# Performance work log

Hardware: AMD Instinct MI355X
Metric: run time of the kernel (lower is better)

The kernel has to match this reference:

```python
import jax, jax.numpy as jnp
import numpy as np

T = 100000
HDIM = 16
UDIM = 7
HID = 64
DT = 5.0 / 60.0  # 5 minutes in hours


def setup_inputs() -> dict:
    key = jax.random.key(0)
    ks = jax.random.split(key, 12)

    def lin(k, out_d, in_d):
        # torch nn.Linear default init: U(-1/sqrt(in), 1/sqrt(in)); scale-equivalent gaussian is fine for a numeric reference
        bound = 1.0 / np.sqrt(in_d)
        return jax.random.uniform(k, (out_d, in_d), jnp.float32, -bound, bound)

    return {
        "U": jax.random.normal(ks[0], (T, UDIM), jnp.float32),
        "W1": lin(ks[1], HID, HDIM + UDIM),
        "b1": jnp.zeros((HID,), jnp.float32),
        "W2": lin(ks[2], HID, HID),
        "b2": jnp.zeros((HID,), jnp.float32),
        "W3": lin(ks[3], HDIM, HID),
        "b3": jnp.zeros((HDIM,), jnp.float32),
        "wd": lin(ks[4], 1, HDIM).reshape(HDIM),
        "bd": jnp.zeros((), jnp.float32),
        "wt": lin(ks[5], 1, HDIM).reshape(HDIM),
        "bt": jnp.zeros((), jnp.float32),
        "wc": lin(ks[6], 1, HDIM).reshape(HDIM),
        "bc": jnp.zeros((), jnp.float32),
        "h0": jnp.zeros((HDIM,), jnp.float32),
    }


def reference(U, W1, b1, W2, b2, W3, b3, wd, bd, wt, bt, wc, bc, h0):
    dt = jnp.float32(DT)

    def step(h, u):
        # readout at current state (before the Euler step), matching the torch loop order
        d = h @ wd + bd
        tx = h @ wt + bt
        ll = h @ wc + bc
        x = jnp.concatenate([h, u])                    # (HDIM+UDIM,)
        z = jnp.tanh(W1 @ x + b1)                      # (HID,)
        z = jnp.tanh(W2 @ z + b2)                      # (HID,)
        dh = W3 @ z + b3                               # (HDIM,)
        return h + dh * dt, (d, tx, ll)

    hT, (delay, taxi, loglam) = jax.lax.scan(step, h0, U)
    return delay, taxi, loglam, hT.reshape(1, HDIM)
```

## Files before the change

### kernel.cpp

```cpp
#include <hip/hip_runtime.h>

typedef float v2f __attribute__((ext_vector_type(2)));

#define T_STEPS 100000
#define UDIM 7
#define NCHUNK 1562
#define TAIL 32
#define ZSTR 68
#define ZH (64 * ZSTR)
#define UROWS 65
#define UAB (UROWS * 64)

__device__ __forceinline__ float tanh_fast(float x) {
    float e = __expf(2.0f * x);
    return 1.0f - 2.0f * __builtin_amdgcn_rcpf(e + 1.0f);
}

__device__ __forceinline__ float readlane_f(float v, int l) {
    return __int_as_float(__builtin_amdgcn_readlane(__float_as_int(v), l));
}

template <int CTRL>
__device__ __forceinline__ float dpp_f(float v) {
    return __int_as_float(__builtin_amdgcn_update_dpp(
        0, __float_as_int(v), CTRL, 0xF, 0xF, true));
}

__global__ __launch_bounds__(128) __attribute__((amdgpu_waves_per_eu(1, 1)))
void node_scan(const float* __restrict__ U,
               const float* __restrict__ W1, const float* __restrict__ b1,
               const float* __restrict__ W2, const float* __restrict__ b2,
               const float* __restrict__ W3, const float* __restrict__ b3,
               const float* __restrict__ wd, const float* __restrict__ bd,
               const float* __restrict__ wt, const float* __restrict__ bt,
               const float* __restrict__ wc, const float* __restrict__ bc,
               const float* __restrict__ h0,
               float* __restrict__ out)
{
    const int tid  = threadIdx.x;
    const int wv   = tid >> 6;
    const int lane = tid & 63;
    const int g = lane >> 2;
    const int q = lane & 3;
    const float dt = (float)(5.0 / 60.0);

    __shared__ __align__(16) float zbuf[64];
    __shared__ __align__(16) float ubuf[3 * 512];
    __shared__ __align__(16) float zhist[2 * ZH];
    __shared__ __align__(16) float cbuf[3 * 64];
    __shared__ __align__(16) float uab[2 * UAB];
    __shared__ __align__(16) float Msh[64 * 64];
    __shared__ int flg[4];

    if (tid == 0) { flg[0] = 0; flg[1] = 0; flg[2] = 0; }

    float w1h[16]; float b2r = 0.f;
    v2f W2p[4][8];
    v2f W1up[3]; float W1u6 = 0.f, b1l = 0.f;
    float rbD = 0.f, rbT = 0.f, rbC = 0.f, rchD = 0.f, rchT = 0.f, rchC = 0.f;

    if (wv == 0) {
#pragma unroll
        for (int j = 0; j < 16; ++j) w1h[j] = W1[lane * 23 + j];
        b2r = b2[lane];
#pragma unroll
        for (int d = 0; d < 4; ++d) {
            const int orow = (g << 2) | (q ^ d);
            const float* w2r = W2 + orow * 64 + q * 16;
#pragma unroll
            for (int j = 0; j < 8; ++j) W2p[d][j] = (v2f){ w2r[2 * j], w2r[2 * j + 1] };
        }
        for (int c = 0; c < 64; ++c) {
            float acc = 0.f;
#pragma unroll
            for (int k = 0; k < 16; ++k) acc = fmaf(w1h[k], W3[k * 64 + c], acc);
            Msh[lane * 64 + c] = acc;
        }
    } else {
#pragma unroll
        for (int j = 0; j < 3; ++j) {
            W1up[j].x = W1[lane * 23 + 16 + 2 * j];
            W1up[j].y = W1[lane * 23 + 17 + 2 * j];
        }
        W1u6 = W1[lane * 23 + 22];
        b1l = b1[lane];
        float cd = 0.f, ct = 0.f, cc = 0.f;
        for (int k = 0; k < 16; ++k) {
            const float w3v = W3[k * 64 + lane];
            cd = fmaf(wd[k], w3v, cd);
            ct = fmaf(wt[k], w3v, ct);
            cc = fmaf(wc[k], w3v, cc);
        }
        cbuf[lane] = cd; cbuf[64 + lane] = ct; cbuf[128 + lane] = cc;
        rchD = bd[0]; rchT = bt[0]; rchC = bc[0];
        for (int k = 0; k < 16; ++k) {
            rbD = fmaf(wd[k], b3[k], rbD);  rchD = fmaf(wd[k], h0[k], rchD);
            rbT = fmaf(wt[k], b3[k], rbT);  rchT = fmaf(wt[k], h0[k], rchT);
            rbC = fmaf(wc[k], b3[k], rbC);  rchC = fmaf(wc[k], h0[k], rchC);
        }
        rbD *= dt; rbT *= dt; rbC *= dt;
#pragma unroll
        for (int c = 0; c < 3; ++c) {
            const int base = c * 448, dst = c * 512;
#pragma unroll
            for (int r = 0; r < UDIM; ++r) {
                int flat = r * 64 + lane;
                int s = flat / 7, cc2 = flat % 7;
                ubuf[dst + s * 8 + cc2] = U[base + flat];
            }
            ubuf[dst + lane * 8 + 7] = 0.f;
        }
    }
    __syncthreads();

    if (wv == 0) {
        v2f Mp[4][8];
#pragma unroll
        for (int d = 0; d < 4; ++d) {
            const int orow = (g << 2) | (q ^ d);
            const float* mr = Msh + orow * 64 + q * 16;
#pragma unroll
            for (int j = 0; j < 8; ++j) Mp[d][j] = (v2f){ mr[2 * j], mr[2 * j + 1] };
        }
        float m3od = 0.f;
#pragma unroll
        for (int k = 0; k < 16; ++k) m3od = fmaf(w1h[k], b3[k], m3od);
        float A = 0.f;
        for (int k = 0; k < 16; ++k) A = fmaf(w1h[k], h0[k], A);

        while (__hip_atomic_load(&flg[1], __ATOMIC_ACQUIRE,
                                 __HIP_MEMORY_SCOPE_WORKGROUP) < 1)
            __builtin_amdgcn_s_sleep(1);
        float uacc = uab[lane];

        auto step = [&](int li, int ub4, int zb4) {
            const float z1 = tanh_fast(A + uacc);
            zbuf[lane] = z1;
            float4 s0 = *(const float4*)&zbuf[q * 16 + 0];
            float4 s1 = *(const float4*)&zbuf[q * 16 + 4];
            float4 s2 = *(const float4*)&zbuf[q * 16 + 8];
            float4 s3 = *(const float4*)&zbuf[q * 16 + 12];
            const float uacc_next = uab[ub4 + (li + 1) * 64 + lane];

            v2f e0 = {s0.x, s0.y}, e1 = {s0.z, s0.w};
            v2f e2 = {s1.x, s1.y}, e3 = {s1.z, s1.w};
            v2f e4 = {s2.x, s2.y}, e5 = {s2.z, s2.w};
            v2f e6 = {s3.x, s3.y}, e7 = {s3.z, s3.w};
            v2f c0 = {b2r, 0.f}, c1 = {0.f, 0.f}, c2 = {0.f, 0.f}, c3 = {0.f, 0.f};
            c0 = __builtin_elementwise_fma(W2p[0][0], e0, c0);
            c1 = __builtin_elementwise_fma(W2p[1][0], e0, c1);
            c2 = __builtin_elementwise_fma(W2p[2][0], e0, c2);
            c3 = __builtin_elementwise_fma(W2p[3][0], e0, c3);
            c0 = __builtin_elementwise_fma(W2p[0][1], e1, c0);
            c1 = __builtin_elementwise_fma(W2p[1][1], e1, c1);
            c2 = __builtin_elementwise_fma(W2p[2][1], e1, c2);
            c3 = __builtin_elementwise_fma(W2p[3][1], e1, c3);
            c0 = __builtin_elementwise_fma(W2p[0][2], e2, c0);
            c1 = __builtin_elementwise_fma(W2p[1][2], e2, c1);
            c2 = __builtin_elementwise_fma(W2p[2][2], e2, c2);
            c3 = __builtin_elementwise_fma(W2p[3][2], e2, c3);
            c0 = __builtin_elementwise_fma(W2p[0][3], e3, c0);
            c1 = __builtin_elementwise_fma(W2p[1][3], e3, c1);
            c2 = __builtin_elementwise_fma(W2p[2][3], e3, c2);
            c3 = __builtin_elementwise_fma(W2p[3][3], e3, c3);
            c0 = __builtin_elementwise_fma(W2p[0][4], e4, c0);
            c1 = __builtin_elementwise_fma(W2p[1][4], e4, c1);
            c2 = __builtin_elementwise_fma(W2p[2][4], e4, c2);
            c3 = __builtin_elementwise_fma(W2p[3][4], e4, c3);
            c0 = __builtin_elementwise_fma(W2p[0][5], e5, c0);
            c1 = __builtin_elementwise_fma(W2p[1][5], e5, c1);
            c2 = __builtin_elementwise_fma(W2p[2][5], e5, c2);
            c3 = __builtin_elementwise_fma(W2p[3][5], e5, c3);
            c0 = __builtin_elementwise_fma(W2p[0][6], e6, c0);
            c1 = __builtin_elementwise_fma(W2p[1][6], e6, c1);
            c2 = __builtin_elementwise_fma(W2p[2][6], e6, c2);
            c3 = __builtin_elementwise_fma(W2p[3][6], e6, c3);
            c0 = __builtin_elementwise_fma(W2p[0][7], e7, c0);
            c1 = __builtin_elementwise_fma(W2p[1][7], e7, c1);
            c2 = __builtin_elementwise_fma(W2p[2][7], e7, c2);
            c3 = __builtin_elementwise_fma(W2p[3][7], e7, c3);
            const float P0 = c0.x + c0.y;
            const float P1 = c1.x + c1.y;
            const float P2 = c2.x + c2.y;
            const float P3 = c3.x + c3.y;
            const float Q = P0 + dpp_f<0xB1>(P1) + dpp_f<0x4E>(P2) + dpp_f<0x1B>(P3);
            const float z2 = tanh_fast(Q);
            zhist[zb4 + li * ZSTR + lane] = z2;
            const float* zrow = &zhist[zb4 + li * ZSTR + q * 16];
            float4 t0 = *(const float4*)&zrow[0];
            float4 t1 = *(const float4*)&zrow[4];
            float4 t2 = *(const float4*)&zrow[8];
            float4 t3 = *(const float4*)&zrow[12];

            v2f f0 = {t0.x, t0.y}, f1 = {t0.z, t0.w};
            v2f f2 = {t1.x, t1.y}, f3 = {t1.z, t1.w};
            v2f f4 = {t2.x, t2.y}, f5 = {t2.z, t2.w};
            v2f f6 = {t3.x, t3.y}, f7 = {t3.z, t3.w};
            v2f m0 = {m3od, 0.f}, m1 = {0.f, 0.f}, m2 = {0.f, 0.f}, m3 = {0.f, 0.f};
            m0 = __builtin_elementwise_fma(Mp[0][0], f0, m0);
            m1 = __builtin_elementwise_fma(Mp[1][0], f0, m1);
            m2 = __builtin_elementwise_fma(Mp[2][0], f0, m2);
            m3 = __builtin_elementwise_fma(Mp[3][0], f0, m3);
            m0 = __builtin_elementwise_fma(Mp[0][1], f1, m0);
            m1 = __builtin_elementwise_fma(Mp[1][1], f1, m1);
            m2 = __builtin_elementwise_fma(Mp[2][1], f1, m2);
            m3 = __builtin_elementwise_fma(Mp[3][1], f1, m3);
            m0 = __builtin_elementwise_fma(Mp[0][2], f2, m0);
            m1 = __builtin_elementwise_fma(Mp[1][2], f2, m1);
            m2 = __builtin_elementwise_fma(Mp[2][2], f2, m2);
            m3 = __builtin_elementwise_fma(Mp[3][2], f2, m3);
            m0 = __builtin_elementwise_fma(Mp[0][3], f3, m0);
            m1 = __builtin_elementwise_fma(Mp[1][3], f3, m1);
            m2 = __builtin_elementwise_fma(Mp[2][3], f3, m2);
            m3 = __builtin_elementwise_fma(Mp[3][3], f3, m3);
            m0 = __builtin_elementwise_fma(Mp[0][4], f4, m0);
            m1 = __builtin_elementwise_fma(Mp[1][4], f4, m1);
            m2 = __builtin_elementwise_fma(Mp[2][4], f4, m2);
            m3 = __builtin_elementwise_fma(Mp[3][4], f4, m3);
            m0 = __builtin_elementwise_fma(Mp[0][5], f5, m0);
            m1 = __builtin_elementwise_fma(Mp[1][5], f5, m1);
            m2 = __builtin_elementwise_fma(Mp[2][5], f5, m2);
            m3 = __builtin_elementwise_fma(Mp[3][5], f5, m3);
            m0 = __builtin_elementwise_fma(Mp[0][6], f6, m0);
            m1 = __builtin_elementwise_fma(Mp[1][6], f6, m1);
            m2 = __builtin_elementwise_fma(Mp[2][6], f6, m2);
            m3 = __builtin_elementwise_fma(Mp[3][6], f6, m3);
            m0 = __builtin_elementwise_fma(Mp[0][7], f7, m0);
            m1 = __builtin_elementwise_fma(Mp[1][7], f7, m1);
            m2 = __builtin_elementwise_fma(Mp[2][7], f7, m2);
            m3 = __builtin_elementwise_fma(Mp[3][7], f7, m3);
            const float R0 = m0.x + m0.y;
            const float R1 = m1.x + m1.y;
            const float R2 = m2.x + m2.y;
            const float R3 = m3.x + m3.y;
            const float R = R0 + dpp_f<0xB1>(R1) + dpp_f<0x4E>(R2) + dpp_f<0x1B>(R3);
            A = fmaf(dt, R, A);
            uacc = uacc_next;
        };

        for (int cb = 0; cb <= NCHUNK; ++cb) {
            while (__hip_atomic_load(&flg[1], __ATOMIC_ACQUIRE,
                                     __HIP_MEMORY_SCOPE_WORKGROUP) < cb + 1)
                __builtin_amdgcn_s_sleep(1);
            while (__hip_atomic_load(&flg[2], __ATOMIC_ACQUIRE,
                                     __HIP_MEMORY_SCOPE_WORKGROUP) < cb - 1)
                __builtin_amdgcn_s_sleep(1);
            const int zb4 = (cb & 1) * ZH;
            const int ub4 = (cb & 1) * UAB;
            if (cb < NCHUNK) {
#pragma unroll 8
                for (int li = 0; li < 64; ++li) step(li, ub4, zb4);
            } else {
                for (int li = 0; li < TAIL; ++li) step(li, ub4, zb4);
            }
            __hip_atomic_store(&flg[0], cb + 1, __ATOMIC_RELEASE,
                               __HIP_MEMORY_SCOPE_WORKGROUP);
        }
    } else {
        float vacc = 0.f;

        auto uacc_chunk = [&](int c) {
            const int par = (c & 1) * UAB;
            const int src = (c % 3) * 512;
            const int nxt = ((c + 1) % 3) * 512;
            for (int li = 0; li < UROWS; ++li) {
                const int uo = (li < 64) ? src + li * 8 : nxt;
                float4 ua = *(const float4*)&ubuf[uo];
                float4 ub = *(const float4*)&ubuf[uo + 4];
                v2f uv = __builtin_elementwise_fma(W1up[0], (v2f){ua.x, ua.y}, (v2f){0.f, 0.f});
                uv = __builtin_elementwise_fma(W1up[1], (v2f){ua.z, ua.w}, uv);
                uv = __builtin_elementwise_fma(W1up[2], (v2f){ub.x, ub.y}, uv);
                uab[par + li * 64 + lane] = uv.x + uv.y + fmaf(W1u6, ub.z, b1l);
            }
        };
        uacc_chunk(0);
        uacc_chunk(1);
        __hip_atomic_store(&flg[1], 2, __ATOMIC_RELEASE,
                           __HIP_MEMORY_SCOPE_WORKGROUP);

        for (int cb = 0; cb <= NCHUNK; ++cb) {
            while (__hip_atomic_load(&flg[0], __ATOMIC_ACQUIRE,
                                     __HIP_MEMORY_SCOPE_WORKGROUP) < cb + 1)
                __builtin_amdgcn_s_sleep(8);
            if (cb + 3 <= NCHUNK) {
                const int dst = ((cb + 3) % 3) * 512;
                const int base = (cb + 3) * 448;
#pragma unroll
                for (int r = 0; r < UDIM; ++r) {
                    int idx = base + r * 64 + lane;
                    if (idx > T_STEPS * UDIM - 1) idx = T_STEPS * UDIM - 1;
                    const float val = U[idx];
                    int flat = r * 64 + lane;
                    int s = flat / 7, c = flat % 7;
                    ubuf[dst + s * 8 + c] = val;
                }
            }
            if (cb + 2 <= NCHUNK) {
                uacc_chunk(cb + 2);
                __hip_atomic_store(&flg[1], cb + 3, __ATOMIC_RELEASE,
                                   __HIP_MEMORY_SCOPE_WORKGROUP);
            }
            const int zb4 = (cb & 1) * ZH;
            const int ns = (cb == NCHUNK) ? TAIL : 64;
            float colsum = 0.f;
            for (int li = 0; li < ns; ++li) colsum += zhist[zb4 + li * ZSTR + lane];
            vacc += colsum;

            const float* zr = &zhist[zb4 + lane * ZSTR];
            v2f sd = {0.f, 0.f}, st = {0.f, 0.f}, sc = {0.f, 0.f};
#pragma unroll
            for (int qq = 0; qq < 32; ++qq) {
                v2f zv = *(const v2f*)&zr[2 * qq];
                sd = __builtin_elementwise_fma(*(const v2f*)&cbuf[2 * qq],       zv, sd);
                st = __builtin_elementwise_fma(*(const v2f*)&cbuf[64 + 2 * qq],  zv, st);
                sc = __builtin_elementwise_fma(*(const v2f*)&cbuf[128 + 2 * qq], zv, sc);
            }
            float Sd = sd.x + sd.y, St = st.x + st.y, Sc = sc.x + sc.y;
            const float oD = Sd, oT = St, oC = Sc;
#pragma unroll
            for (int dl = 1; dl < 64; dl <<= 1) {
                float ud = __shfl_up(Sd, dl, 64);
                float ut = __shfl_up(St, dl, 64);
                float uc = __shfl_up(Sc, dl, 64);
                if (lane >= dl) { Sd += ud; St += ut; Sc += uc; }
            }
            const int t = cb * 64 + lane;
            if (t < T_STEPS) {
                const float fl = (float)lane;
                out[t]               = fmaf(dt, Sd - oD, rchD) + fl * rbD;
                out[T_STEPS + t]     = fmaf(dt, St - oT, rchT) + fl * rbT;
                out[2 * T_STEPS + t] = fmaf(dt, Sc - oC, rchC) + fl * rbC;
            }
            rchD = fmaf(dt, readlane_f(Sd, 63), rchD) + 64.f * rbD;
            rchT = fmaf(dt, readlane_f(St, 63), rchT) + 64.f * rbT;
            rchC = fmaf(dt, readlane_f(Sc, 63), rchC) + 64.f * rbC;
            __hip_atomic_store(&flg[2], cb + 1, __ATOMIC_RELEASE,
                               __HIP_MEMORY_SCOPE_WORKGROUP);
        }

        zbuf[lane] = vacc;
        if (lane < 16) {
            const float* w3r = W3 + lane * 64;
            float h0a = 0.f, h1a = 0.f;
#pragma unroll
            for (int qq = 0; qq < 16; ++qq) {
                float4 za = *(const float4*)&zbuf[qq * 4];
                h0a = fmaf(w3r[4 * qq + 0], za.x, h0a);
                h1a = fmaf(w3r[4 * qq + 1], za.y, h1a);
                h0a = fmaf(w3r[4 * qq + 2], za.z, h0a);
                h1a = fmaf(w3r[4 * qq + 3], za.w, h1a);
            }
            out[3 * T_STEPS + lane] =
                h0[lane] + dt * (h0a + h1a) + (float)T_STEPS * dt * b3[lane];
        }
    }
}

extern "C" void kernel_launch(void* const* d_in, const int* in_sizes, int n_in,
                              void* d_out, int out_size, void* d_ws, size_t ws_size,
                              hipStream_t stream) {
    const float* U  = (const float*)d_in[0];
    const float* W1 = (const float*)d_in[1];
    const float* b1 = (const float*)d_in[2];
    const float* W2 = (const float*)d_in[3];
    const float* b2 = (const float*)d_in[4];
    const float* W3 = (const float*)d_in[5];
    const float* b3 = (const float*)d_in[6];
    const float* wd = (const float*)d_in[7];
    const float* bd = (const float*)d_in[8];
    const float* wt = (const float*)d_in[9];
    const float* bt = (const float*)d_in[10];
    const float* wc = (const float*)d_in[11];
    const float* bc = (const float*)d_in[12];
    const float* h0 = (const float*)d_in[13];
    (void)in_sizes; (void)n_in; (void)out_size; (void)d_ws; (void)ws_size;

    node_scan<<<dim3(1), dim3(128), 0, stream>>>(U, W1, b1, W2, b2, W3, b3,
                                                 wd, bd, wt, bt, wc, bc, h0,
                                                 (float*)d_out);
}
```

Measured before the change: 26.39 ms.

## Replace LDS broadcast of hidden state with DPP row rotations and permlane-swap reductions

Restructures the serial per-step matvecs so each lane keeps a 16-wide row slice and rotates activations within 16-lane rows via DPP instead of writing z1 to LDS and reading it back. Cross-row partial sums are combined with permlane32/16 swaps when available (probed at runtime), with a bpermute/swizzle fallback. The factor of two in tanh's argument is folded into the weights. This aims to shorten the latency-bound per-step critical path by removing LDS round trips, at the cost of extra DPP instructions and a runtime mode check.

```diff
diff --git a/kernel.cpp b/kernel.cpp
--- a/kernel.cpp
+++ b/kernel.cpp
@@ -11,8 +11,14 @@
 #define UROWS 65
 #define UAB (UROWS * 64)
 
-__device__ __forceinline__ float tanh_fast(float x) {
-    float e = __expf(2.0f * x);
+#if __has_builtin(__builtin_amdgcn_permlane32_swap) && __has_builtin(__builtin_amdgcn_permlane16_swap)
+#define HAS_PLSWAP 1
+#else
+#define HAS_PLSWAP 0
+#endif
+
+__device__ __forceinline__ float tanh_pre(float xs) {
+    float e = __expf(xs);
     return 1.0f - 2.0f * __builtin_amdgcn_rcpf(e + 1.0f);
 }
 
@@ -25,6 +31,8 @@
     return __int_as_float(__builtin_amdgcn_update_dpp(
         0, __float_as_int(v), CTRL, 0xF, 0xF, true));
 }
+
+template <int M> struct IC { static constexpr int v = M; };
 
 __global__ __launch_bounds__(128) __attribute__((amdgpu_waves_per_eu(1, 1)))
 void node_scan(const float* __restrict__ U,
@@ -40,8 +48,6 @@
     const int tid  = threadIdx.x;
     const int wv   = tid >> 6;
     const int lane = tid & 63;
-    const int g = lane >> 2;
-    const int q = lane & 3;
     const float dt = (float)(5.0 / 60.0);
 
     __shared__ __align__(16) float zbuf[64];
@@ -54,44 +60,60 @@
 
     if (tid == 0) { flg[0] = 0; flg[1] = 0; flg[2] = 0; }
 
-    float w1h[16]; float b2r = 0.f;
-    v2f W2p[4][8];
+    int dlt = 1, mode = 1;
+    float A = 0.f, m3od = 0.f;
     v2f W1up[3]; float W1u6 = 0.f, b1l = 0.f;
     float rbD = 0.f, rbT = 0.f, rbC = 0.f, rchD = 0.f, rchT = 0.f, rchC = 0.f;
 
     if (wv == 0) {
-#pragma unroll
-        for (int j = 0; j < 16; ++j) w1h[j] = W1[lane * 23 + j];
-        b2r = b2[lane];
-#pragma unroll
-        for (int d = 0; d < 4; ++d) {
-            const int orow = (g << 2) | (q ^ d);
-            const float* w2r = W2 + orow * 64 + q * 16;
-#pragma unroll
-            for (int j = 0; j < 8; ++j) W2p[d][j] = (v2f){ w2r[2 * j], w2r[2 * j + 1] };
-        }
-        for (int c = 0; c < 64; ++c) {
+        const int cl = lane & 15;
+        {
+            float pd = dpp_f<0x121>((float)cl);
+            dlt = ((int)pd - cl) & 15;
+        }
+#if HAS_PLSWAP
+        {
+            auto rp = __builtin_amdgcn_permlane32_swap(lane, 1000 + lane, false, false);
+            auto rq = __builtin_amdgcn_permlane16_swap(lane, 1000 + lane, false, false);
+            bool ok =
+                (int)rp[0] == ((lane & 32) ? 1000 + lane - 32 : lane) &&
+                (int)rp[1] == ((lane & 32) ? 1000 + lane : lane + 32) &&
+                (int)rq[0] == ((lane & 16) ? 1000 + lane - 16 : lane) &&
+                (int)rq[1] == ((lane & 16) ? 1000 + lane : lane + 16);
+            if (__ballot(ok) == ~0ull) mode = 0;
+        }
+#endif
+        float w1h[16];
+#pragma unroll
+        for (int j = 0; j < 16; ++j) w1h[j] = 2.0f * W1[lane * 23 + j];
+        for (int cc = 0; cc < 64; ++cc) {
             float acc = 0.f;
 #pragma unroll
-            for (int k = 0; k < 16; ++k) acc = fmaf(w1h[k], W3[k * 64 + c], acc);
-            Msh[lane * 64 + c] = acc;
-        }
+            for (int k = 0; k < 16; ++k) acc = fmaf(w1h[k], W3[k * 64 + cc], acc);
+            Msh[lane * 64 + cc] = acc;
+        }
+#pragma unroll
+        for (int k = 0; k < 16; ++k) {
+            m3od = fmaf(w1h[k], b3[k], m3od);
+            A    = fmaf(w1h[k], h0[k], A);
+        }
+        zbuf[lane] = m3od;
     } else {
 #pragma unroll
         for (int j = 0; j < 3; ++j) {
-            W1up[j].x = W1[lane * 23 + 16 + 2 * j];
-            W1up[j].y = W1[lane * 23 + 17 + 2 * j];
-        }
-        W1u6 = W1[lane * 23 + 22];
-        b1l = b1[lane];
-        float cd = 0.f, ct = 0.f, cc = 0.f;
+            W1up[j].x = 2.0f * W1[lane * 23 + 16 + 2 * j];
+            W1up[j].y = 2.0f * W1[lane * 23 + 17 + 2 * j];
+        }
+        W1u6 = 2.0f * W1[lane * 23 + 22];
+        b1l = 2.0f * b1[lane];
+        float cd = 0.f, ct = 0.f, ccv = 0.f;
         for (int k = 0; k < 16; ++k) {
             const float w3v = W3[k * 64 + lane];
             cd = fmaf(wd[k], w3v, cd);
             ct = fmaf(wt[k], w3v, ct);
-            cc = fmaf(wc[k], w3v, cc);
-        }
-        cbuf[lane] = cd; cbuf[64 + lane] = ct; cbuf[128 + lane] = cc;
+            ccv = fmaf(wc[k], w3v, ccv);
+        }
+        cbuf[lane] = cd; cbuf[64 + lane] = ct; cbuf[128 + lane] = ccv;
         rchD = bd[0]; rchT = bt[0]; rchC = bc[0];
         for (int k = 0; k < 16; ++k) {
             rbD = fmaf(wd[k], b3[k], rbD);  rchD = fmaf(wd[k], h0[k], rchD);
@@ -103,8 +125,8 @@
         for (int c = 0; c < 3; ++c) {
             const int base = c * 448, dst = c * 512;
 #pragma unroll
-            for (int r = 0; r < UDIM; ++r) {
-                int flat = r * 64 + lane;
+            for (int rr = 0; rr < UDIM; ++rr) {
+                int flat = rr * 64 + lane;
                 int s = flat / 7, cc2 = flat % 7;
                 ubuf[dst + s * 8 + cc2] = U[base + flat];
             }
@@ -114,148 +136,120 @@
     __syncthreads();
 
     if (wv == 0) {
-        v2f Mp[4][8];
-#pragma unroll
-        for (int d = 0; d < 4; ++d) {
-            const int orow = (g << 2) | (q ^ d);
-            const float* mr = Msh + orow * 64 + q * 16;
-#pragma unroll
-            for (int j = 0; j < 8; ++j) Mp[d][j] = (v2f){ mr[2 * j], mr[2 * j + 1] };
-        }
-        float m3od = 0.f;
-#pragma unroll
-        for (int k = 0; k < 16; ++k) m3od = fmaf(w1h[k], b3[k], m3od);
-        float A = 0.f;
-        for (int k = 0; k < 16; ++k) A = fmaf(w1h[k], h0[k], A);
-
-        while (__hip_atomic_load(&flg[1], __ATOMIC_ACQUIRE,
-                                 __HIP_MEMORY_SCOPE_WORKGROUP) < 1)
-            __builtin_amdgcn_s_sleep(1);
-        float uacc = uab[lane];
-
-        auto step = [&](int li, int ub4, int zb4) {
-            const float z1 = tanh_fast(A + uacc);
-            zbuf[lane] = z1;
-            float4 s0 = *(const float4*)&zbuf[q * 16 + 0];
-            float4 s1 = *(const float4*)&zbuf[q * 16 + 4];
-            float4 s2 = *(const float4*)&zbuf[q * 16 + 8];
-            float4 s3 = *(const float4*)&zbuf[q * 16 + 12];
-            const float uacc_next = uab[ub4 + (li + 1) * 64 + lane];
-
-            v2f e0 = {s0.x, s0.y}, e1 = {s0.z, s0.w};
-            v2f e2 = {s1.x, s1.y}, e3 = {s1.z, s1.w};
-            v2f e4 = {s2.x, s2.y}, e5 = {s2.z, s2.w};
-            v2f e6 = {s3.x, s3.y}, e7 = {s3.z, s3.w};
-            v2f c0 = {b2r, 0.f}, c1 = {0.f, 0.f}, c2 = {0.f, 0.f}, c3 = {0.f, 0.f};
-            c0 = __builtin_elementwise_fma(W2p[0][0], e0, c0);
-            c1 = __builtin_elementwise_fma(W2p[1][0], e0, c1);
-            c2 = __builtin_elementwise_fma(W2p[2][0], e0, c2);
-            c3 = __builtin_elementwise_fma(W2p[3][0], e0, c3);
-            c0 = __builtin_elementwise_fma(W2p[0][1], e1, c0);
-            c1 = __builtin_elementwise_fma(W2p[1][1], e1, c1);
-            c2 = __builtin_elementwise_fma(W2p[2][1], e1, c2);
-            c3 = __builtin_elementwise_fma(W2p[3][1], e1, c3);
-            c0 = __builtin_elementwise_fma(W2p[0][2], e2, c0);
-            c1 = __builtin_elementwise_fma(W2p[1][2], e2, c1);
-            c2 = __builtin_elementwise_fma(W2p[2][2], e2, c2);
-            c3 = __builtin_elementwise_fma(W2p[3][2], e2, c3);
-            c0 = __builtin_elementwise_fma(W2p[0][3], e3, c0);
-            c1 = __builtin_elementwise_fma(W2p[1][3], e3, c1);
-            c2 = __builtin_elementwise_fma(W2p[2][3], e3, c2);
-            c3 = __builtin_elementwise_fma(W2p[3][3], e3, c3);
-            c0 = __builtin_elementwise_fma(W2p[0][4], e4, c0);
-            c1 = __builtin_elementwise_fma(W2p[1][4], e4, c1);
-            c2 = __builtin_elementwise_fma(W2p[2][4], e4, c2);
-            c3 = __builtin_elementwise_fma(W2p[3][4], e4, c3);
-            c0 = __builtin_elementwise_fma(W2p[0][5], e5, c0);
-            c1 = __builtin_elementwise_fma(W2p[1][5], e5, c1);
-            c2 = __builtin_elementwise_fma(W2p[2][5], e5, c2);
-            c3 = __builtin_elementwise_fma(W2p[3][5], e5, c3);
-            c0 = __builtin_elementwise_fma(W2p[0][6], e6, c0);
-            c1 = __builtin_elementwise_fma(W2p[1][6], e6, c1);
-            c2 = __builtin_elementwise_fma(W2p[2][6], e6, c2);
-            c3 = __builtin_elementwise_fma(W2p[3][6], e6, c3);
-            c0 = __builtin_elementwise_fma(W2p[0][7], e7, c0);
-            c1 = __builtin_elementwise_fma(W2p[1][7], e7, c1);
-            c2 = __builtin_elementwise_fma(W2p[2][7], e7, c2);
-            c3 = __builtin_elementwise_fma(W2p[3][7], e7, c3);
-            const float P0 = c0.x + c0.y;
-            const float P1 = c1.x + c1.y;
-            const float P2 = c2.x + c2.y;
-            const float P3 = c3.x + c3.y;
-            const float Q = P0 + dpp_f<0xB1>(P1) + dpp_f<0x4E>(P2) + dpp_f<0x1B>(P3);
-            const float z2 = tanh_fast(Q);
-            zhist[zb4 + li * ZSTR + lane] = z2;
-            const float* zrow = &zhist[zb4 + li * ZSTR + q * 16];
-            float4 t0 = *(const float4*)&zrow[0];
-            float4 t1 = *(const float4*)&zrow[4];
-            float4 t2 = *(const float4*)&zrow[8];
-            float4 t3 = *(const float4*)&zrow[12];
-
-            v2f f0 = {t0.x, t0.y}, f1 = {t0.z, t0.w};
-            v2f f2 = {t1.x, t1.y}, f3 = {t1.z, t1.w};
-            v2f f4 = {t2.x, t2.y}, f5 = {t2.z, t2.w};
-            v2f f6 = {t3.x, t3.y}, f7 = {t3.z, t3.w};
-            v2f m0 = {m3od, 0.f}, m1 = {0.f, 0.f}, m2 = {0.f, 0.f}, m3 = {0.f, 0.f};
-            m0 = __builtin_elementwise_fma(Mp[0][0], f0, m0);
-            m1 = __builtin_elementwise_fma(Mp[1][0], f0, m1);
-            m2 = __builtin_elementwise_fma(Mp[2][0], f0, m2);
-            m3 = __builtin_elementwise_fma(Mp[3][0], f0, m3);
-            m0 = __builtin_elementwise_fma(Mp[0][1], f1, m0);
-            m1 = __builtin_elementwise_fma(Mp[1][1], f1, m1);
-            m2 = __builtin_elementwise_fma(Mp[2][1], f1, m2);
-            m3 = __builtin_elementwise_fma(Mp[3][1], f1, m3);
-            m0 = __builtin_elementwise_fma(Mp[0][2], f2, m0);
-            m1 = __builtin_elementwise_fma(Mp[1][2], f2, m1);
-            m2 = __builtin_elementwise_fma(Mp[2][2], f2, m2);
-            m3 = __builtin_elementwise_fma(Mp[3][2], f2, m3);
-            m0 = __builtin_elementwise_fma(Mp[0][3], f3, m0);
-            m1 = __builtin_elementwise_fma(Mp[1][3], f3, m1);
-            m2 = __builtin_elementwise_fma(Mp[2][3], f3, m2);
-            m3 = __builtin_elementwise_fma(Mp[3][3], f3, m3);
-            m0 = __builtin_elementwise_fma(Mp[0][4], f4, m0);
-            m1 = __builtin_elementwise_fma(Mp[1][4], f4, m1);
-            m2 = __builtin_elementwise_fma(Mp[2][4], f4, m2);
-            m3 = __builtin_elementwise_fma(Mp[3][4], f4, m3);
-            m0 = __builtin_elementwise_fma(Mp[0][5], f5, m0);
-            m1 = __builtin_elementwise_fma(Mp[1][5], f5, m1);
-            m2 = __builtin_elementwise_fma(Mp[2][5], f5, m2);
-            m3 = __builtin_elementwise_fma(Mp[3][5], f5, m3);
-            m0 = __builtin_elementwise_fma(Mp[0][6], f6, m0);
-            m1 = __builtin_elementwise_fma(Mp[1][6], f6, m1);
-            m2 = __builtin_elementwise_fma(Mp[2][6], f6, m2);
-            m3 = __builtin_elementwise_fma(Mp[3][6], f6, m3);
-            m0 = __builtin_elementwise_fma(Mp[0][7], f7, m0);
-            m1 = __builtin_elementwise_fma(Mp[1][7], f7, m1);
-            m2 = __builtin_elementwise_fma(Mp[2][7], f7, m2);
-            m3 = __builtin_elementwise_fma(Mp[3][7], f7, m3);
-            const float R0 = m0.x + m0.y;
-            const float R1 = m1.x + m1.y;
-            const float R2 = m2.x + m2.y;
-            const float R3 = m3.x + m3.y;
-            const float R = R0 + dpp_f<0xB1>(R1) + dpp_f<0x4E>(R2) + dpp_f<0x1B>(R3);
-            A = fmaf(dt, R, A);
-            uacc = uacc_next;
+        const int r  = lane >> 4;
+        const int cl = lane & 15;
+
+        auto runw0 = [&](auto MC) {
+            constexpr int MODE = decltype(MC)::v;
+            v2f W2f[4][8], Mf[4][8];
+            float b2v[4], m3v[4];
+            {
+                int offA = 0, offB = (15 * dlt) & 15;
+#pragma unroll
+                for (int s = 0; s < 8; ++s) {
+                    const int kA = (r << 4) | ((cl + offA) & 15);
+                    const int kB = (r << 4) | ((cl + offB) & 15);
+#pragma unroll
+                    for (int d = 0; d < 4; ++d) {
+                        const int o = ((MODE ? (r ^ d) : d) << 4) | cl;
+                        W2f[d][s] = (v2f){2.0f * W2[o * 64 + kA], 2.0f * W2[o * 64 + kB]};
+                        Mf[d][s]  = (v2f){Msh[o * 64 + kA], Msh[o * 64 + kB]};
+                    }
+                    offA = (offA + 2 * dlt) & 15;
+                    offB = (offB + 2 * dlt) & 15;
+                }
+#pragma unroll
+                for (int d = 0; d < 4; ++d) {
+                    if (MODE == 0) {
+                        b2v[d] = (r == 0) ? 2.0f * b2[(d << 4) | cl] : 0.f;
+                        m3v[d] = (r == 0) ? zbuf[(d << 4) | cl] : 0.f;
+                    } else {
+                        b2v[d] = (d == 0) ? 2.0f * b2[lane] : 0.f;
+                        m3v[d] = (d == 0) ? m3od : 0.f;
+                    }
+                }
+            }
+
+            auto combine = [&](v2f a0, v2f a1, v2f a2, v2f a3) -> float {
+                float P0 = a0.x + a0.y, P1 = a1.x + a1.y;
+                float P2 = a2.x + a2.y, P3 = a3.x + a3.y;
+#if HAS_PLSWAP
+                if constexpr (MODE == 0) {
+                    auto rA = __builtin_amdgcn_permlane32_swap(__float_as_int(P0), __float_as_int(P2), false, false);
+                    auto rB = __builtin_amdgcn_permlane32_swap(__float_as_int(P1), __float_as_int(P3), false, false);
+                    float U02 = __int_as_float((int)rA[0]) + __int_as_float((int)rA[1]);
+                    float U13 = __int_as_float((int)rB[0]) + __int_as_float((int)rB[1]);
+                    auto sA = __builtin_amdgcn_permlane16_swap(__float_as_int(U02), __float_as_int(U02), false, false);
+                    auto sB = __builtin_amdgcn_permlane16_swap(__float_as_int(U13), __float_as_int(U13), false, false);
+                    float V02 = __int_as_float((int)sA[0]) + __int_as_float((int)sA[1]);
+                    float V13 = __int_as_float((int)sB[0]) + __int_as_float((int)sB[1]);
+                    return (lane & 16) ? V13 : V02;
+                }
+#endif
+                {
+                    float q0 = P0 + __int_as_float(__builtin_amdgcn_ds_bpermute((lane ^ 32) << 2, __float_as_int(P2)));
+                    float q1 = P1 + __int_as_float(__builtin_amdgcn_ds_bpermute((lane ^ 32) << 2, __float_as_int(P3)));
+                    return q0 + __int_as_float(__builtin_amdgcn_ds_swizzle(__float_as_int(q1), 0x401F));
+                }
+            };
+
+            while (__hip_atomic_load(&flg[1], __ATOMIC_ACQUIRE,
+                                     __HIP_MEMORY_SCOPE_WORKGROUP) < 1)
+                __builtin_amdgcn_s_sleep(1);
+            float uacc = uab[lane];
+
+            auto step = [&](int li, int ub4, int zb4) {
+                const float z1 = tanh_pre(A + uacc);
+                const float uacc_next = uab[ub4 + (li + 1) * 64 + lane];
+                v2f zp; zp.x = z1; zp.y = dpp_f<0x12F>(z1);
+                v2f a0 = {b2v[0], 0.f}, a1 = {b2v[1], 0.f};
+                v2f a2 = {b2v[2], 0.f}, a3 = {b2v[3], 0.f};
+#pragma unroll
+                for (int s = 0; s < 8; ++s) {
+                    a0 = __builtin_elementwise_fma(W2f[0][s], zp, a0);
+                    a1 = __builtin_elementwise_fma(W2f[1][s], zp, a1);
+                    a2 = __builtin_elementwise_fma(W2f[2][s], zp, a2);
+                    a3 = __builtin_elementwise_fma(W2f[3][s], zp, a3);
+                    if (s < 7) { zp.x = dpp_f<0x122>(zp.x); zp.y = dpp_f<0x122>(zp.y); }
+                }
+                const float z2 = tanh_pre(combine(a0, a1, a2, a3));
+                zhist[zb4 + li * ZSTR + lane] = z2;
+                v2f wp; wp.x = z2; wp.y = dpp_f<0x12F>(z2);
+                v2f m0 = {m3v[0], 0.f}, m1 = {m3v[1], 0.f};
+                v2f m2 = {m3v[2], 0.f}, m3r = {m3v[3], 0.f};
+#pragma unroll
+                for (int s = 0; s < 8; ++s) {
+                    m0  = __builtin_elementwise_fma(Mf[0][s], wp, m0);
+                    m1  = __builtin_elementwise_fma(Mf[1][s], wp, m1);
+                    m2  = __builtin_elementwise_fma(Mf[2][s], wp, m2);
+                    m3r = __builtin_elementwise_fma(Mf[3][s], wp, m3r);
+                    if (s < 7) { wp.x = dpp_f<0x122>(wp.x); wp.y = dpp_f<0x122>(wp.y); }
+                }
+                A = fmaf(dt, combine(m0, m1, m2, m3r), A);
+                uacc = uacc_next;
+            };
+
+            for (int cb = 0; cb <= NCHUNK; ++cb) {
+                while (__hip_atomic_load(&flg[1], __ATOMIC_ACQUIRE,
+                                         __HIP_MEMORY_SCOPE_WORKGROUP) < cb + 1)
+                    __builtin_amdgcn_s_sleep(1);
+                while (__hip_atomic_load(&flg[2], __ATOMIC_ACQUIRE,
+                                         __HIP_MEMORY_SCOPE_WORKGROUP) < cb - 1)
+                    __builtin_amdgcn_s_sleep(1);
+                const int zb4 = (cb & 1) * ZH;
+                const int ub4 = (cb & 1) * UAB;
+                if (cb < NCHUNK) {
+#pragma unroll 4
+                    for (int li = 0; li < 64; ++li) step(li, ub4, zb4);
+                } else {
+#pragma unroll 4
+                    for (int li = 0; li < TAIL; ++li) step(li, ub4, zb4);
+                }
+                __hip_atomic_store(&flg[0], cb + 1, __ATOMIC_RELEASE,
+                                   __HIP_MEMORY_SCOPE_WORKGROUP);
+            }
         };
-
-        for (int cb = 0; cb <= NCHUNK; ++cb) {
-            while (__hip_atomic_load(&flg[1], __ATOMIC_ACQUIRE,
-                                     __HIP_MEMORY_SCOPE_WORKGROUP) < cb + 1)
-                __builtin_amdgcn_s_sleep(1);
-            while (__hip_atomic_load(&flg[2], __ATOMIC_ACQUIRE,
-                                     __HIP_MEMORY_SCOPE_WORKGROUP) < cb - 1)
-                __builtin_amdgcn_s_sleep(1);
-            const int zb4 = (cb & 1) * ZH;
-            const int ub4 = (cb & 1) * UAB;
-            if (cb < NCHUNK) {
-#pragma unroll 8
-                for (int li = 0; li < 64; ++li) step(li, ub4, zb4);
-            } else {
-                for (int li = 0; li < TAIL; ++li) step(li, ub4, zb4);
-            }
-            __hip_atomic_store(&flg[0], cb + 1, __ATOMIC_RELEASE,
-                               __HIP_MEMORY_SCOPE_WORKGROUP);
-        }
+        if (mode == 0) runw0(IC<0>{}); else runw0(IC<1>{});
     } else {
         float vacc = 0.f;
 
@@ -286,11 +280,11 @@
                 const int dst = ((cb + 3) % 3) * 512;
                 const int base = (cb + 3) * 448;
 #pragma unroll
-                for (int r = 0; r < UDIM; ++r) {
-                    int idx = base + r * 64 + lane;
+                for (int rr = 0; rr < UDIM; ++rr) {
+                    int idx = base + rr * 64 + lane;
                     if (idx > T_STEPS * UDIM - 1) idx = T_STEPS * UDIM - 1;
                     const float val = U[idx];
-                    int flat = r * 64 + lane;
+                    int flat = rr * 64 + lane;
                     int s = flat / 7, c = flat % 7;
                     ubuf[dst + s * 8 + c] = val;
                 }
```

New measurement: 28.41 ms. +7.6%, slower.

## Fold tanh doubling and dt into weights, rebalance reductions, raise wave priority

Applied to the files above, without the earlier changes.

Pre-scales W1, b1, W2 and b2 by 2 so each tanh skips a multiply, and folds dt into the precomputed M matrix and bias so the state update becomes a plain add. Precomputes A+u ahead of the next step. Reassociates the DPP reduction sums into a tree to shorten the dependency chain on the serial critical path. Raises the compute wave's scheduling priority and widens the readout loop to float4 LDS loads. This slightly changes floating-point rounding.

```diff
diff --git a/kernel.cpp b/kernel.cpp
--- a/kernel.cpp
+++ b/kernel.cpp
@@ -11,8 +11,8 @@
 #define UROWS 65
 #define UAB (UROWS * 64)
 
-__device__ __forceinline__ float tanh_fast(float x) {
-    float e = __expf(2.0f * x);
+__device__ __forceinline__ float tanh_pre(float xs) {
+    float e = __expf(xs);
     return 1.0f - 2.0f * __builtin_amdgcn_rcpf(e + 1.0f);
 }
 
@@ -61,14 +61,15 @@
 
     if (wv == 0) {
 #pragma unroll
-        for (int j = 0; j < 16; ++j) w1h[j] = W1[lane * 23 + j];
-        b2r = b2[lane];
+        for (int j = 0; j < 16; ++j) w1h[j] = 2.0f * W1[lane * 23 + j];
+        b2r = 2.0f * b2[lane];
 #pragma unroll
         for (int d = 0; d < 4; ++d) {
             const int orow = (g << 2) | (q ^ d);
             const float* w2r = W2 + orow * 64 + q * 16;
 #pragma unroll
-            for (int j = 0; j < 8; ++j) W2p[d][j] = (v2f){ w2r[2 * j], w2r[2 * j + 1] };
+            for (int j = 0; j < 8; ++j)
+                W2p[d][j] = (v2f){ 2.0f * w2r[2 * j], 2.0f * w2r[2 * j + 1] };
         }
         for (int c = 0; c < 64; ++c) {
             float acc = 0.f;
@@ -79,11 +80,11 @@
     } else {
 #pragma unroll
         for (int j = 0; j < 3; ++j) {
-            W1up[j].x = W1[lane * 23 + 16 + 2 * j];
-            W1up[j].y = W1[lane * 23 + 17 + 2 * j];
-        }
-        W1u6 = W1[lane * 23 + 22];
-        b1l = b1[lane];
+            W1up[j].x = 2.0f * W1[lane * 23 + 16 + 2 * j];
+            W1up[j].y = 2.0f * W1[lane * 23 + 17 + 2 * j];
+        }
+        W1u6 = 2.0f * W1[lane * 23 + 22];
+        b1l = 2.0f * b1[lane];
         float cd = 0.f, ct = 0.f, cc = 0.f;
         for (int k = 0; k < 16; ++k) {
             const float w3v = W3[k * 64 + lane];
@@ -114,27 +115,30 @@
     __syncthreads();
 
     if (wv == 0) {
+        __builtin_amdgcn_s_setprio(3);
         v2f Mp[4][8];
 #pragma unroll
         for (int d = 0; d < 4; ++d) {
             const int orow = (g << 2) | (q ^ d);
             const float* mr = Msh + orow * 64 + q * 16;
 #pragma unroll
-            for (int j = 0; j < 8; ++j) Mp[d][j] = (v2f){ mr[2 * j], mr[2 * j + 1] };
+            for (int j = 0; j < 8; ++j)
+                Mp[d][j] = (v2f){ dt * mr[2 * j], dt * mr[2 * j + 1] };
         }
         float m3od = 0.f;
 #pragma unroll
         for (int k = 0; k < 16; ++k) m3od = fmaf(w1h[k], b3[k], m3od);
+        m3od *= dt;
         float A = 0.f;
         for (int k = 0; k < 16; ++k) A = fmaf(w1h[k], h0[k], A);
 
         while (__hip_atomic_load(&flg[1], __ATOMIC_ACQUIRE,
                                  __HIP_MEMORY_SCOPE_WORKGROUP) < 1)
             __builtin_amdgcn_s_sleep(1);
-        float uacc = uab[lane];
+        float Az = A + uab[lane];
 
         auto step = [&](int li, int ub4, int zb4) {
-            const float z1 = tanh_fast(A + uacc);
+            const float z1 = tanh_pre(Az);
             zbuf[lane] = z1;
             float4 s0 = *(const float4*)&zbuf[q * 16 + 0];
             float4 s1 = *(const float4*)&zbuf[q * 16 + 4];
@@ -183,8 +187,8 @@
             const float P1 = c1.x + c1.y;
             const float P2 = c2.x + c2.y;
             const float P3 = c3.x + c3.y;
-            const float Q = P0 + dpp_f<0xB1>(P1) + dpp_f<0x4E>(P2) + dpp_f<0x1B>(P3);
-            const float z2 = tanh_fast(Q);
+            const float Q = (P0 + dpp_f<0xB1>(P1)) + (dpp_f<0x4E>(P2) + dpp_f<0x1B>(P3));
+            const float z2 = tanh_pre(Q);
             zhist[zb4 + li * ZSTR + lane] = z2;
             const float* zrow = &zhist[zb4 + li * ZSTR + q * 16];
             float4 t0 = *(const float4*)&zrow[0];
@@ -233,9 +237,9 @@
             const float R1 = m1.x + m1.y;
             const float R2 = m2.x + m2.y;
             const float R3 = m3.x + m3.y;
-            const float R = R0 + dpp_f<0xB1>(R1) + dpp_f<0x4E>(R2) + dpp_f<0x1B>(R3);
-            A = fmaf(dt, R, A);
-            uacc = uacc_next;
+            const float R = (R0 + dpp_f<0xB1>(R1)) + (dpp_f<0x4E>(R2) + dpp_f<0x1B>(R3));
+            A = A + R;
+            Az = A + uacc_next;
         };
 
         for (int cb = 0; cb <= NCHUNK; ++cb) {
@@ -309,11 +313,18 @@
             const float* zr = &zhist[zb4 + lane * ZSTR];
             v2f sd = {0.f, 0.f}, st = {0.f, 0.f}, sc = {0.f, 0.f};
 #pragma unroll
-            for (int qq = 0; qq < 32; ++qq) {
-                v2f zv = *(const v2f*)&zr[2 * qq];
-                sd = __builtin_elementwise_fma(*(const v2f*)&cbuf[2 * qq],       zv, sd);
-                st = __builtin_elementwise_fma(*(const v2f*)&cbuf[64 + 2 * qq],  zv, st);
-                sc = __builtin_elementwise_fma(*(const v2f*)&cbuf[128 + 2 * qq], zv, sc);
+            for (int qq = 0; qq < 16; ++qq) {
+                float4 zv4 = *(const float4*)&zr[4 * qq];
+                float4 cd4 = *(const float4*)&cbuf[4 * qq];
+                float4 ct4 = *(const float4*)&cbuf[64 + 4 * qq];
+                float4 cc4 = *(const float4*)&cbuf[128 + 4 * qq];
+                v2f zlo = {zv4.x, zv4.y}, zhi = {zv4.z, zv4.w};
+                sd = __builtin_elementwise_fma((v2f){cd4.x, cd4.y}, zlo, sd);
+                sd = __builtin_elementwise_fma((v2f){cd4.z, cd4.w}, zhi, sd);
+                st = __builtin_elementwise_fma((v2f){ct4.x, ct4.y}, zlo, st);
+                st = __builtin_elementwise_fma((v2f){ct4.z, ct4.w}, zhi, st);
+                sc = __builtin_elementwise_fma((v2f){cc4.x, cc4.y}, zlo, sc);
+                sc = __builtin_elementwise_fma((v2f){cc4.z, cc4.w}, zhi, sc);
             }
             float Sd = sd.x + sd.y, St = st.x + st.y, Sc = sc.x + sc.y;
             const float oD = Sd, oT = St, oC = Sc;
```

New measurement: 26.66 ms. Within noise of the previous version (+1.0%).

## Replace LDS broadcast of hidden activations with permlane/DPP butterfly exchange

Applied to the files above, without the earlier changes.

On the serial recurrence wave, each step used to broadcast z1 and z2 through LDS (a store followed by float4 reloads). Where the permlane32/16 swap builtins exist, it now gathers 16 values per lane with cross-lane permutes and DPP row rotates. The W2 and M weight registers are permuted to match, and a runtime check confirms the gathered indices cover the quad, falling back to the LDS path otherwise. The aim is to cut LDS round-trip latency from the critical dependency chain, at the cost of more permute instructions and code duplication.

```diff
diff --git a/kernel.cpp b/kernel.cpp
--- a/kernel.cpp
+++ b/kernel.cpp
@@ -11,6 +11,12 @@
 #define UROWS 65
 #define UAB (UROWS * 64)
 
+#if __has_builtin(__builtin_amdgcn_permlane32_swap) && __has_builtin(__builtin_amdgcn_permlane16_swap)
+#define HAS_PLSWAP 1
+#else
+#define HAS_PLSWAP 0
+#endif
+
 __device__ __forceinline__ float tanh_fast(float x) {
     float e = __expf(2.0f * x);
     return 1.0f - 2.0f * __builtin_amdgcn_rcpf(e + 1.0f);
@@ -25,6 +31,28 @@
     return __int_as_float(__builtin_amdgcn_update_dpp(
         0, __float_as_int(v), CTRL, 0xF, 0xF, true));
 }
+
+template <int CTRL>
+__device__ __forceinline__ int dpp_i(int v) {
+    return __builtin_amdgcn_update_dpp(0, v, CTRL, 0xF, 0xF, true);
+}
+
+#if HAS_PLSWAP
+__device__ __forceinline__ void bfly16(int v, int c[16]) {
+    auto p  = __builtin_amdgcn_permlane32_swap(v, v, false, false);
+    auto qa = __builtin_amdgcn_permlane16_swap(p[0], p[0], false, false);
+    auto qb = __builtin_amdgcn_permlane16_swap(p[1], p[1], false, false);
+    int a0 = qa[0], a1 = qa[1], a2 = qb[0], a3 = qb[1];
+    int b0 = dpp_i<0x128>(a0), b1 = dpp_i<0x128>(a1);
+    int b2 = dpp_i<0x128>(a2), b3 = dpp_i<0x128>(a3);
+    c[0] = a0;  c[1] = a1;  c[2] = a2;  c[3] = a3;
+    c[4] = b0;  c[5] = b1;  c[6] = b2;  c[7] = b3;
+    c[8]  = dpp_i<0x124>(a0);  c[9]  = dpp_i<0x124>(a1);
+    c[10] = dpp_i<0x124>(a2);  c[11] = dpp_i<0x124>(a3);
+    c[12] = dpp_i<0x124>(b0);  c[13] = dpp_i<0x124>(b1);
+    c[14] = dpp_i<0x124>(b2);  c[15] = dpp_i<0x124>(b3);
+}
+#endif
 
 __global__ __launch_bounds__(128) __attribute__((amdgpu_waves_per_eu(1, 1)))
 void node_scan(const float* __restrict__ U,
@@ -56,19 +84,48 @@
 
     float w1h[16]; float b2r = 0.f;
     v2f W2p[4][8];
+    int idx[16]; bool fastok = false;
     v2f W1up[3]; float W1u6 = 0.f, b1l = 0.f;
     float rbD = 0.f, rbT = 0.f, rbC = 0.f, rchD = 0.f, rchT = 0.f, rchC = 0.f;
 
     if (wv == 0) {
+#if HAS_PLSWAP
+        {
+            int c[16];
+            bfly16(lane, c);
+            unsigned mlo = 0, mhi = 0;
+#pragma unroll
+            for (int r = 0; r < 16; ++r) {
+                idx[r] = c[r] & 63;
+                if (idx[r] < 32) mlo |= (1u << idx[r]);
+                else             mhi |= (1u << (idx[r] - 32));
+            }
+            unsigned ulo = mlo, uhi = mhi;
+            ulo |= (unsigned)dpp_i<0xB1>((int)mlo);
+            ulo |= (unsigned)dpp_i<0x4E>((int)mlo);
+            ulo |= (unsigned)dpp_i<0x1B>((int)mlo);
+            uhi |= (unsigned)dpp_i<0xB1>((int)mhi);
+            uhi |= (unsigned)dpp_i<0x4E>((int)mhi);
+            uhi |= (unsigned)dpp_i<0x1B>((int)mhi);
+            bool ok = (ulo == 0xFFFFFFFFu) && (uhi == 0xFFFFFFFFu);
+            fastok = (__ballot(ok) == ~0ull);
+        }
+#endif
+        if (!fastok) {
+#pragma unroll
+            for (int r = 0; r < 16; ++r) idx[r] = (q << 4) | r;
+        }
+
 #pragma unroll
         for (int j = 0; j < 16; ++j) w1h[j] = W1[lane * 23 + j];
         b2r = b2[lane];
 #pragma unroll
         for (int d = 0; d < 4; ++d) {
             const int orow = (g << 2) | (q ^ d);
-            const float* w2r = W2 + orow * 64 + q * 16;
-#pragma unroll
-            for (int j = 0; j < 8; ++j) W2p[d][j] = (v2f){ w2r[2 * j], w2r[2 * j + 1] };
+            const float* w2r = W2 + orow * 64;
+#pragma unroll
+            for (int j = 0; j < 8; ++j)
+                W2p[d][j] = (v2f){ w2r[idx[2 * j]], w2r[idx[2 * j + 1]] };
         }
         for (int c = 0; c < 64; ++c) {
             float acc = 0.f;
@@ -118,9 +175,10 @@
 #pragma unroll
         for (int d = 0; d < 4; ++d) {
             const int orow = (g << 2) | (q ^ d);
-            const float* mr = Msh + orow * 64 + q * 16;
-#pragma unroll
-            for (int j = 0; j < 8; ++j) Mp[d][j] = (v2f){ mr[2 * j], mr[2 * j + 1] };
+            const float* mr = Msh + orow * 64;
+#pragma unroll
+            for (int j = 0; j < 8; ++j)
+                Mp[d][j] = (v2f){ mr[idx[2 * j]], mr[idx[2 * j + 1]] };
         }
         float m3od = 0.f;
 #pragma unroll
@@ -133,19 +191,8 @@
             __builtin_amdgcn_s_sleep(1);
         float uacc = uab[lane];
 
-        auto step = [&](int li, int ub4, int zb4) {
-            const float z1 = tanh_fast(A + uacc);
-            zbuf[lane] = z1;
-            float4 s0 = *(const float4*)&zbuf[q * 16 + 0];
-            float4 s1 = *(const float4*)&zbuf[q * 16 + 4];
-            float4 s2 = *(const float4*)&zbuf[q * 16 + 8];
-            float4 s3 = *(const float4*)&zbuf[q * 16 + 12];
-            const float uacc_next = uab[ub4 + (li + 1) * 64 + lane];
-
-            v2f e0 = {s0.x, s0.y}, e1 = {s0.z, s0.w};
-            v2f e2 = {s1.x, s1.y}, e3 = {s1.z, s1.w};
-            v2f e4 = {s2.x, s2.y}, e5 = {s2.z, s2.w};
-            v2f e6 = {s3.x, s3.y}, e7 = {s3.z, s3.w};
+        auto mat2 = [&](v2f e0, v2f e1, v2f e2, v2f e3,
+                        v2f e4, v2f e5, v2f e6, v2f e7) -> float {
             v2f c0 = {b2r, 0.f}, c1 = {0.f, 0.f}, c2 = {0.f, 0.f}, c3 = {0.f, 0.f};
             c0 = __builtin_elementwise_fma(W2p[0][0], e0, c0);
             c1 = __builtin_elementwise_fma(W2p[1][0], e0, c1);
@@ -183,19 +230,10 @@
             const float P1 = c1.x + c1.y;
             const float P2 = c2.x + c2.y;
             const float P3 = c3.x + c3.y;
-            const float Q = P0 + dpp_f<0xB1>(P1) + dpp_f<0x4E>(P2) + dpp_f<0x1B>(P3);
-            const float z2 = tanh_fast(Q);
-            zhist[zb4 + li * ZSTR + lane] = z2;
-            const float* zrow = &zhist[zb4 + li * ZSTR + q * 16];
-            float4 t0 = *(const float4*)&zrow[0];
-            float4 t1 = *(const float4*)&zrow[4];
-            float4 t2 = *(const float4*)&zrow[8];
-            float4 t3 = *(const float4*)&zrow[12];
-
-            v2f f0 = {t0.x, t0.y}, f1 = {t0.z, t0.w};
-            v2f f2 = {t1.x, t1.y}, f3 = {t1.z, t1.w};
-            v2f f4 = {t2.x, t2.y}, f5 = {t2.z, t2.w};
-            v2f f6 = {t3.x, t3.y}, f7 = {t3.z, t3.w};
+            return P0 + dpp_f<0xB1>(P1) + dpp_f<0x4E>(P2) + dpp_f<0x1B>(P3);
+        };
+        auto mat3 = [&](v2f f0, v2f f1, v2f f2, v2f f3,
+                        v2f f4, v2f f5, v2f f6, v2f f7) -> float {
             v2f m0 = {m3od, 0.f}, m1 = {0.f, 0.f}, m2 = {0.f, 0.f}, m3 = {0.f, 0.f};
             m0 = __builtin_elementwise_fma(Mp[0][0], f0, m0);
             m1 = __builtin_elementwise_fma(Mp[1][0], f0, m1);
@@ -233,28 +271,109 @@
             const float R1 = m1.x + m1.y;
             const float R2 = m2.x + m2.y;
             const float R3 = m3.x + m3.y;
-            const float R = R0 + dpp_f<0xB1>(R1) + dpp_f<0x4E>(R2) + dpp_f<0x1B>(R3);
+            return R0 + dpp_f<0xB1>(R1) + dpp_f<0x4E>(R2) + dpp_f<0x1B>(R3);
+        };
+
+#if HAS_PLSWAP
+        auto stepF = [&](int li, int ub4, int zb4) {
+            const float z1 = tanh_fast(A + uacc);
+            const float uacc_next = uab[ub4 + (li + 1) * 64 + lane];
+            int zg[16];
+            bfly16(__float_as_int(z1), zg);
+            const float Q = mat2(
+                (v2f){__int_as_float(zg[0]),  __int_as_float(zg[1])},
+                (v2f){__int_as_float(zg[2]),  __int_as_float(zg[3])},
+                (v2f){__int_as_float(zg[4]),  __int_as_float(zg[5])},
+                (v2f){__int_as_float(zg[6]),  __int_as_float(zg[7])},
+                (v2f){__int_as_float(zg[8]),  __int_as_float(zg[9])},
+                (v2f){__int_as_float(zg[10]), __int_as_float(zg[11])},
+                (v2f){__int_as_float(zg[12]), __int_as_float(zg[13])},
+                (v2f){__int_as_float(zg[14]), __int_as_float(zg[15])});
+            const float z2 = tanh_fast(Q);
+            zhist[zb4 + li * ZSTR + lane] = z2;
+            int wg[16];
+            bfly16(__float_as_int(z2), wg);
+            const float R = mat3(
+                (v2f){__int_as_float(wg[0]),  __int_as_float(wg[1])},
+                (v2f){__int_as_float(wg[2]),  __int_as_float(wg[3])},
+                (v2f){__int_as_float(wg[4]),  __int_as_float(wg[5])},
+                (v2f){__int_as_float(wg[6]),  __int_as_float(wg[7])},
+                (v2f){__int_as_float(wg[8]),  __int_as_float(wg[9])},
+                (v2f){__int_as_float(wg[10]), __int_as_float(wg[11])},
+                (v2f){__int_as_float(wg[12]), __int_as_float(wg[13])},
+                (v2f){__int_as_float(wg[14]), __int_as_float(wg[15])});
             A = fmaf(dt, R, A);
             uacc = uacc_next;
         };
-
-        for (int cb = 0; cb <= NCHUNK; ++cb) {
-            while (__hip_atomic_load(&flg[1], __ATOMIC_ACQUIRE,
-                                     __HIP_MEMORY_SCOPE_WORKGROUP) < cb + 1)
-                __builtin_amdgcn_s_sleep(1);
-            while (__hip_atomic_load(&flg[2], __ATOMIC_ACQUIRE,
-                                     __HIP_MEMORY_SCOPE_WORKGROUP) < cb - 1)
-                __builtin_amdgcn_s_sleep(1);
-            const int zb4 = (cb & 1) * ZH;
-            const int ub4 = (cb & 1) * UAB;
-            if (cb < NCHUNK) {
+#endif
+        auto stepS = [&](int li, int ub4, int zb4) {
+            const float z1 = tanh_fast(A + uacc);
+            zbuf[lane] = z1;
+            float4 s0 = *(const float4*)&zbuf[q * 16 + 0];
+            float4 s1 = *(const float4*)&zbuf[q * 16 + 4];
+            float4 s2 = *(const float4*)&zbuf[q * 16 + 8];
+            float4 s3 = *(const float4*)&zbuf[q * 16 + 12];
+            const float uacc_next = uab[ub4 + (li + 1) * 64 + lane];
+            const float Q = mat2((v2f){s0.x, s0.y}, (v2f){s0.z, s0.w},
+                                 (v2f){s1.x, s1.y}, (v2f){s1.z, s1.w},
+                                 (v2f){s2.x, s2.y}, (v2f){s2.z, s2.w},
+                                 (v2f){s3.x, s3.y}, (v2f){s3.z, s3.w});
+            const float z2 = tanh_fast(Q);
+            zhist[zb4 + li * ZSTR + lane] = z2;
+            const float* zrow = &zhist[zb4 + li * ZSTR + q * 16];
+            float4 t0 = *(const float4*)&zrow[0];
+            float4 t1 = *(const float4*)&zrow[4];
+            float4 t2 = *(const float4*)&zrow[8];
+            float4 t3 = *(const float4*)&zrow[12];
+            const float R = mat3((v2f){t0.x, t0.y}, (v2f){t0.z, t0.w},
+                                 (v2f){t1.x, t1.y}, (v2f){t1.z, t1.w},
+                                 (v2f){t2.x, t2.y}, (v2f){t2.z, t2.w},
+                                 (v2f){t3.x, t3.y}, (v2f){t3.z, t3.w});
+            A = fmaf(dt, R, A);
+            uacc = uacc_next;
+        };
+
+#if HAS_PLSWAP
+        if (fastok) {
+            for (int cb = 0; cb <= NCHUNK; ++cb) {
+                while (__hip_atomic_load(&flg[1], __ATOMIC_ACQUIRE,
+                                         __HIP_MEMORY_SCOPE_WORKGROUP) < cb + 1)
+                    __builtin_amdgcn_s_sleep(1);
+                while (__hip_atomic_load(&flg[2], __ATOMIC_ACQUIRE,
+                                         __HIP_MEMORY_SCOPE_WORKGROUP) < cb - 1)
+                    __builtin_amdgcn_s_sleep(1);
+                const int zb4 = (cb & 1) * ZH;
+                const int ub4 = (cb & 1) * UAB;
+                if (cb < NCHUNK) {
 #pragma unroll 8
-                for (int li = 0; li < 64; ++li) step(li, ub4, zb4);
-            } else {
-                for (int li = 0; li < TAIL; ++li) step(li, ub4, zb4);
-            }
-            __hip_atomic_store(&flg[0], cb + 1, __ATOMIC_RELEASE,
-                               __HIP_MEMORY_SCOPE_WORKGROUP);
+                    for (int li = 0; li < 64; ++li) stepF(li, ub4, zb4);
+                } else {
+                    for (int li = 0; li < TAIL; ++li) stepF(li, ub4, zb4);
+                }
+                __hip_atomic_store(&flg[0], cb + 1, __ATOMIC_RELEASE,
+                                   __HIP_MEMORY_SCOPE_WORKGROUP);
+            }
+        } else
+#endif
+        {
+            for (int cb = 0; cb <= NCHUNK; ++cb) {
+                while (__hip_atomic_load(&flg[1], __ATOMIC_ACQUIRE,
+                                         __HIP_MEMORY_SCOPE_WORKGROUP) < cb + 1)
+                    __builtin_amdgcn_s_sleep(1);
+                while (__hip_atomic_load(&flg[2], __ATOMIC_ACQUIRE,
+                                         __HIP_MEMORY_SCOPE_WORKGROUP) < cb - 1)
+                    __builtin_amdgcn_s_sleep(1);
+                const int zb4 = (cb & 1) * ZH;
+                const int ub4 = (cb & 1) * UAB;
+                if (cb < NCHUNK) {
+#pragma unroll 8
+                    for (int li = 0; li < 64; ++li) stepS(li, ub4, zb4);
+                } else {
+                    for (int li = 0; li < TAIL; ++li) stepS(li, ub4, zb4);
+                }
+                __hip_atomic_store(&flg[0], cb + 1, __ATOMIC_RELEASE,
+                                   __HIP_MEMORY_SCOPE_WORKGROUP);
+            }
         }
     } else {
         float vacc = 0.f;
@@ -287,9 +406,9 @@
                 const int base = (cb + 3) * 448;
 #pragma unroll
                 for (int r = 0; r < UDIM; ++r) {
-                    int idx = base + r * 64 + lane;
-                    if (idx > T_STEPS * UDIM - 1) idx = T_STEPS * UDIM - 1;
-                    const float val = U[idx];
+                    int idx2 = base + r * 64 + lane;
+                    if (idx2 > T_STEPS * UDIM - 1) idx2 = T_STEPS * UDIM - 1;
+                    const float val = U[idx2];
                     int flat = r * 64 + lane;
                     int s = flat / 7, c = flat % 7;
                     ubuf[dst + s * 8 + c] = val;
```

New measurement: 29.58 ms. 12.1% more time.
